# Kernel optimization log

Measured on AMD Instinct MI355X. Metric: run time of the kernel, lower is better.

Reference implementation:

```python
import jax, jax.numpy as jnp
import numpy as np

B, D0 = 1, 32
C = [32, 16, 16, 16]
DN = ('NDHWC', 'DHWIO', 'NDHWC')


def setup_inputs() -> dict:
    key = jax.random.key(0)
    ks = jax.random.split(key, 16)
    w = lambda k, s: jax.random.normal(k, s, jnp.float32) * 0.05
    occ0 = jax.random.bernoulli(ks[0], 0.3, (B, D0, D0, D0))
    x = jax.random.normal(ks[1], (B, D0, D0, D0, C[0]), jnp.float32) * occ0[..., None]
    gt0 = jax.random.bernoulli(ks[2], 0.3, (B, D0, D0, D0))
    gt1 = jax.random.bernoulli(ks[3], 0.3, (B, 2 * D0, 2 * D0, 2 * D0))
    gt2 = jax.random.bernoulli(ks[4], 0.3, (B, 4 * D0, 4 * D0, 4 * D0))
    return dict(
        x=x, occ0=occ0, gt0=gt0, gt1=gt1, gt2=gt2,
        w_conv0=w(ks[5], (3, 3, 3, C[0], C[1])), b_conv0=w(ks[6], (C[1],)),
        w_cls0=w(ks[7], (3, 3, 3, C[1], 1)), b_cls0=w(ks[8], (1,)),
        w_up1=w(ks[9], (2, 2, 2, C[1], C[2])), b_up1=w(ks[10], (C[2],)),
        w_conv1=w(ks[11], (3, 3, 3, C[2], C[2])), b_conv1=w(ks[12], (C[2],)),
        w_cls1=w(ks[13], (3, 3, 3, C[2], 1)), b_cls1=w(ks[14], (1,)),
        w_up2=w(jax.random.fold_in(key, 100), (2, 2, 2, C[2], C[3])), b_up2=w(jax.random.fold_in(key, 101), (C[3],)),
        w_conv2=w(jax.random.fold_in(key, 102), (3, 3, 3, C[3], C[3])), b_conv2=w(jax.random.fold_in(key, 103), (C[3],)),
        w_cls2=w(jax.random.fold_in(key, 104), (3, 3, 3, C[3], 1)), b_cls2=w(jax.random.fold_in(key, 105), (1,)),
        nums0=8192, nums1=32768, nums2=131072)


def conv3x3(x, w, b, occ):
    # stride-1 sparse conv == dense conv masked to existing coords
    y = jax.lax.conv_general_dilated(x, w, (1, 1, 1), 'SAME', dimension_numbers=DN)
    return (y + b) * occ[..., None].astype(y.dtype)


def up2x(x, w, b, occ):
    # generative transpose conv: every occupied voxel emits all 8 children
    y = jax.lax.conv_transpose(x, w, (2, 2, 2), 'VALID', dimension_numbers=DN)
    occ_up = jnp.repeat(jnp.repeat(jnp.repeat(occ, 2, 1), 2, 2), 2, 3)
    return (y + b) * occ_up[..., None].astype(y.dtype), occ_up


def prune(feats, occ, cls_logits, gt, k):
    # istopk over existing voxels, OR-ed with ground-truth membership (training=True)
    b = feats.shape[0]
    logits = jnp.where(occ, cls_logits[..., 0], -jnp.inf).reshape(b, -1)
    _, idx = jax.lax.top_k(logits, k)
    topk = jnp.zeros(logits.shape, bool).at[jnp.arange(b)[:, None], idx].set(True)
    mask = (topk.reshape(occ.shape) & occ) | (gt & occ)
    return feats * mask[..., None].astype(feats.dtype), mask


def hp_decoder(x, occ0, gt0, gt1, gt2,
               w_conv0, b_conv0, w_cls0, b_cls0,
               w_up1, b_up1, w_conv1, b_conv1, w_cls1, b_cls1,
               w_up2, b_up2, w_conv2, b_conv2, w_cls2, b_cls2,
               nums0, nums1, nums2):
    occ = occ0
    out = jax.nn.relu(conv3x3(x, w_conv0, b_conv0, occ))
    cls0 = conv3x3(out, w_cls0, b_cls0, occ)
    out, occ = prune(out, occ, cls0, gt0, nums0)
    h, occ = up2x(out, w_up1, b_up1, occ)
    out = jax.nn.relu(conv3x3(jax.nn.relu(h), w_conv1, b_conv1, occ))
    cls1 = conv3x3(out, w_cls1, b_cls1, occ)
    out, occ = prune(out, occ, cls1, gt1, nums1)
    h, occ = up2x(out, w_up2, b_up2, occ)
    out = jax.nn.relu(conv3x3(jax.nn.relu(h), w_conv2, b_conv2, occ))
    cls2 = conv3x3(out, w_cls2, b_cls2, occ)
    out, occ = prune(out, occ, cls2, gt2, nums2)
    return cls0, cls1, cls2, out


def reference(x, occ0, gt0, gt1, gt2,
              w_conv0, b_conv0, w_cls0, b_cls0,
              w_up1, b_up1, w_conv1, b_conv1, w_cls1, b_cls1,
              w_up2, b_up2, w_conv2, b_conv2, w_cls2, b_cls2,
              nums0, nums1, nums2):
    return hp_decoder(x, occ0, gt0, gt1, gt2,
                      w_conv0, b_conv0, w_cls0, b_cls0,
                      w_up1, b_up1, w_conv1, b_conv1, w_cls1, b_cls1,
                      w_up2, b_up2, w_conv2, b_conv2, w_cls2, b_cls2,
                      nums0, nums1, nums2)
```

## Files before the change

### kernel.cpp

```cpp
#include <hip/hip_runtime.h>
#include <stdint.h>


#define N0 32768
#define N1 262144
#define N2 2097152

#define OFF_CLS0 0L
#define OFF_CLS1 32768L
#define OFF_CLS2 294912L
#define OFF_OUT  2392064L

#define O_FLAGS 0UL
#define O_STATE 256UL
#define O_TIE   512UL
#define O_HIST1 66048UL
#define O_HIST2 328192UL
#define O_OCC0  590336UL
#define O_OCC1  623104UL
#define O_OCC2  885248UL
#define O_MASK0 2982400UL
#define O_MASK1 3015168UL
#define O_BCNT  3277312UL
#define O_SEL   5374464UL
#define O_KEYS  7471616UL
#define O_FEAT0 15860224UL
#define O_HR1   17957376UL
#define O_FEAT1 34734592UL
#define O_HR2   51511808UL
#define O_FEAT2 185729536UL

#define TIE_CAP 16000

__device__ __forceinline__ float ldf(const void* p, long i, int bf) {
    if (bf) {
        uint16_t h = ((const uint16_t*)p)[i];
        return __uint_as_float(((uint32_t)h) << 16);
    }
    return ((const float*)p)[i];
}
__device__ __forceinline__ int ldb(const void* p, long i, int m) {
    switch (m) {
        case 0: return ((const int*)p)[i] != 0;
        case 1: return ((const uint8_t*)p)[i] != 0;
        case 2: { uint16_t h = ((const uint16_t*)p)[i]; return (h & 0x7FFF) != 0; }
        case 4: return ((const long long*)p)[i] != 0;
        default: { float f = ((const float*)p)[i]; return f != 0.0f; }
    }
}
__device__ __forceinline__ float rndb(float f, int en) {
    if (!en) return f;
    uint32_t u = __float_as_uint(f);
    u += 0x7FFFu + ((u >> 16) & 1u);
    u &= 0xFFFF0000u;
    return __uint_as_float(u);
}
__device__ __forceinline__ void stf(void* p, long i, float v, int bf) {
    if (bf) {
        uint32_t u = __float_as_uint(v);
        u += 0x7FFFu + ((u >> 16) & 1u);
        ((uint16_t*)p)[i] = (uint16_t)(u >> 16);
    } else {
        ((float*)p)[i] = v;
    }
}
__device__ __forceinline__ uint32_t fkey(float f) {
    f = f + 0.0f;
    uint32_t u = __float_as_uint(f);
    return (u & 0x80000000u) ? ~u : (u | 0x80000000u);
}

__global__ void k_fzero(int* flags) {
    int t = threadIdx.x;
    if (t < 16) flags[8 + t] = 0;
}
__global__ void k_fscan(const void* x, const void* gt2, int* flags) {
    int* cnt = flags + 8;
    __shared__ int lc[8];
    int t = threadIdx.x;
    if (t < 8) lc[t] = 0;
    __syncthreads();
    long gid = (long)blockIdx.x * blockDim.x + threadIdx.x;
    long gstride = (long)gridDim.x * blockDim.x;
    int ltiny = 0;
    const uint32_t* xu = (const uint32_t*)x;
    for (long i = gid; i < 524288; i += gstride) {
        uint32_t u = xu[i];
        uint32_t e = (u >> 23) & 0xFFu;
        if (e == 0u && (u & 0x7FFFFFu) != 0u) ltiny++;
    }
    int l1off = 0, l1any = 0, l3f = 0, l84 = 0;
    const uint8_t* g = (const uint8_t*)gt2;
    for (long i = gid; i < 2097152; i += gstride) {
        uint8_t b = g[i];
        if (b == 1u) {
            l1any++;
            if ((i & 3) != 0) l1off++;
            if ((i & 7) == 4) l84++;
        }
        if (b == 0x3Fu && (i & 3) == 1) l3f++;
    }
    if (ltiny) atomicAdd(&lc[0], ltiny);
    if (l1off) atomicAdd(&lc[1], l1off);
    if (l1any) atomicAdd(&lc[2], l1any);
    if (l3f)   atomicAdd(&lc[3], l3f);
    if (l84)   atomicAdd(&lc[4], l84);
    __syncthreads();
    if (t < 5 && lc[t]) atomicAdd(&cnt[t], lc[t]);
}
__global__ void k_ffinal(int* flags) {
    if (threadIdx.x != 0 || blockIdx.x != 0) return;
    const int* cnt = flags + 8;
    flags[0] = (cnt[0] > 8) ? 1 : 0;
    int bm;
    if (cnt[1] > 8)       bm = 1;
    else if (cnt[2] > 8)  bm = (cnt[4] > 8) ? 0 : 4;
    else if (cnt[3] > 8)  bm = 2;
    else                  bm = 3;
    flags[1] = bm;
}

__global__ void k_zout(void* dout, long out_elems, const int* flags) {
    long bytes = out_elems * (flags[0] ? 2 : 4);
    long n16 = bytes >> 4;
    uint4 z = make_uint4(0, 0, 0, 0);
    uint4* p = (uint4*)dout;
    long stride = (long)gridDim.x * blockDim.x;
    for (long i = (long)blockIdx.x * blockDim.x + threadIdx.x; i < n16; i += stride)
        p[i] = z;
}

__global__ void k_xcast(const void* x, float* xf, const int* flags) {
    long i = (long)blockIdx.x * blockDim.x + threadIdx.x;
    if (i >= (long)N0 * 32) return;
    xf[i] = ldf(x, i, flags[0]);
}

__global__ void k_occ0cnt(const void* occraw, uint8_t* occ, const int* flags,
                          int* __restrict__ bcnt, uint8_t* maskz) {
    long v = (long)blockIdx.x * 256 + threadIdx.x;
    int a = (v < N0) ? ldb(occraw, v, flags[1]) : 0;
    if (v < N0) { occ[v] = (uint8_t)a; maskz[v] = 0; }
    unsigned long long m = __ballot(a != 0);
    __shared__ int wsum[4];
    int lane = threadIdx.x & 63, wid = threadIdx.x >> 6;
    if (lane == 0) wsum[wid] = (int)__popcll(m);
    __syncthreads();
    if (threadIdx.x == 0)
        bcnt[blockIdx.x] = wsum[0] + wsum[1] + wsum[2] + wsum[3];
}
template <int Dp>
__global__ void k_expcnt(const uint8_t* __restrict__ maskp, uint8_t* __restrict__ occc,
                         int* __restrict__ bcnt, uint8_t* maskz) {
    const int D = Dp * 2;
    long v = (long)blockIdx.x * 256 + threadIdx.x;
    const long N = (long)D * D * D;
    int a = 0;
    if (v < N) {
        int wd = (int)(v % D), hh = (int)((v / D) % D), dd = (int)(v / ((long)D * D));
        a = maskp[((long)(dd >> 1) * Dp + (hh >> 1)) * Dp + (wd >> 1)];
        occc[v] = (uint8_t)a;
        if (maskz) maskz[v] = 0;
    }
    unsigned long long m = __ballot(a != 0);
    __shared__ int wsum[4];
    int lane = threadIdx.x & 63, wid = threadIdx.x >> 6;
    if (lane == 0) wsum[wid] = (int)__popcll(m);
    __syncthreads();
    if (threadIdx.x == 0)
        bcnt[blockIdx.x] = wsum[0] + wsum[1] + wsum[2] + wsum[3];
}
__global__ void k_scanb(int* __restrict__ bcnt, int nb, int* cnt) {
    __shared__ int tsum[256];
    __shared__ int tpre[257];
    int t = threadIdx.x;
    int ch = (nb + 255) / 256;
    int lo = t * ch, hi = min(lo + ch, nb);
    int s = 0;
    for (int i = lo; i < hi; i++) s += bcnt[i];
    tsum[t] = s;
    __syncthreads();
    if (t == 0) {
        int run = 0;
        for (int j = 0; j < 256; j++) { tpre[j] = run; run += tsum[j]; }
        tpre[256] = run;
        cnt[0] = run;
    }
    __syncthreads();
    int run = tpre[t];
    for (int i = lo; i < hi; i++) { int x = bcnt[i]; bcnt[i] = run; run += x; }
}
__global__ void k_fill(const uint8_t* __restrict__ occ, long N,
                       const int* __restrict__ bcnt, int* __restrict__ list,
                       uint32_t* __restrict__ h1z) {
    long v = (long)blockIdx.x * 256 + threadIdx.x;
    for (long j = v; j < 65536; j += (long)gridDim.x * 256) h1z[j] = 0u;
    int a = (v < N) && occ[v];
    unsigned long long m = __ballot(a != 0);
    __shared__ int wsum[4];
    int lane = threadIdx.x & 63, wid = threadIdx.x >> 6;
    if (lane == 0) wsum[wid] = (int)__popcll(m);
    __syncthreads();
    int base = bcnt[blockIdx.x];
    for (int w = 0; w < wid; w++) base += wsum[w];
    if (a) list[base + (int)__popcll(m & ((1ull << lane) - 1ull))] = (int)v;
}

template <int CIN, int D>
__global__ void k_sconv16(const float* __restrict__ xin, const void* w, const void* bias,
                          const uint8_t* __restrict__ occ, const int* __restrict__ list,
                          const int* __restrict__ cnt, float* __restrict__ out,
                          const int* __restrict__ flags) {
    __shared__ float wl[27 * CIN * 16 + 16];
    const int n = cnt[0];
    if (blockIdx.x * 128 >= n) return;
    const int bf = flags[0];
    for (int i = threadIdx.x; i < 27 * CIN * 16; i += 256) wl[i] = ldf(w, i, bf);
    if (threadIdx.x < 16) wl[27 * CIN * 16 + threadIdx.x] = ldf(bias, threadIdx.x, bf);
    __syncthreads();
    int gid = blockIdx.x * 256 + threadIdx.x;
    int i = gid >> 1;
    if (i >= n) return;
    const int half = gid & 1;
    int v = list[i];
    int wd = v % D, hh = (v / D) % D, dd = v / (D * D);
    uint32_t nbm = 0u;
    {
        int t = 0;
#pragma unroll
        for (int kd = 0; kd < 3; kd++)
#pragma unroll
            for (int kh = 0; kh < 3; kh++)
#pragma unroll
                for (int kw = 0; kw < 3; kw++, t++) {
                    int d2 = dd + kd - 1, h2 = hh + kh - 1, w2 = wd + kw - 1;
                    int ok = (int)((unsigned)d2 < (unsigned)D) &
                             (int)((unsigned)h2 < (unsigned)D) &
                             (int)((unsigned)w2 < (unsigned)D);
                    int nv = v + (kd - 1) * D * D + (kh - 1) * D + (kw - 1);
                    int nvc = ok ? nv : v;
                    nbm |= ((uint32_t)((int)occ[nvc] & ok)) << t;
                }
    }
    float acc[8];
#pragma unroll
    for (int co = 0; co < 8; co++) acc[co] = 0.0f;
    int t = 0;
    for (int kd = 0; kd < 3; kd++) {
        for (int kh = 0; kh < 3; kh++) {
            for (int kw = 0; kw < 3; kw++, t++) {
                if (!((nbm >> t) & 1u)) continue;
                long nv = (long)v + (kd - 1) * (D * D) + (kh - 1) * D + (kw - 1);
                const float4* xp = (const float4*)(xin + nv * CIN);
                const float* wp = &wl[((kd * 3 + kh) * 3 + kw) * CIN * 16 + half * 8];
#pragma unroll
                for (int c4 = 0; c4 < CIN / 4; c4++) {
                    float4 x4 = xp[c4];
                    const float* wq = wp + c4 * 64;
#pragma unroll
                    for (int co = 0; co < 8; co++) acc[co] += x4.x * wq[co];
#pragma unroll
                    for (int co = 0; co < 8; co++) acc[co] += x4.y * wq[16 + co];
#pragma unroll
                    for (int co = 0; co < 8; co++) acc[co] += x4.z * wq[32 + co];
#pragma unroll
                    for (int co = 0; co < 8; co++) acc[co] += x4.w * wq[48 + co];
                }
            }
        }
    }
    float* op = out + (long)v * 16 + half * 8;
    const float* bp = &wl[27 * CIN * 16 + half * 8];
#pragma unroll
    for (int co = 0; co < 8; co++) {
        float val = rndb(acc[co], bf);
        val = rndb(val + bp[co], bf);
        op[co] = fmaxf(val, 0.0f);
    }
}

template <int D>
__global__ void k_scls(const float* __restrict__ feat, const void* w, const void* bias,
                       const uint8_t* __restrict__ occ, const int* __restrict__ list,
                       const int* __restrict__ cnt, void* dout, long ooff,
                       uint32_t* __restrict__ keyl, const int* __restrict__ flags) {
    __shared__ float wl[27 * 16 + 1];
    const int n = cnt[0];
    if (blockIdx.x * 128 >= n) return;
    const int bf = flags[0];
    for (int i = threadIdx.x; i < 27 * 16; i += 256) wl[i] = ldf(w, i, bf);
    if (threadIdx.x == 0) wl[432] = ldf(bias, 0, bf);
    __syncthreads();
    int gid = blockIdx.x * 256 + threadIdx.x;
    int i = gid >> 1;
    if (i >= n) return;
    const int half = gid & 1;
    int v = list[i];
    int wd = v % D, hh = (v / D) % D, dd = v / (D * D);
    uint32_t nbm = 0u;
    {
        int t = 0;
#pragma unroll
        for (int kd = 0; kd < 3; kd++)
#pragma unroll
            for (int kh = 0; kh < 3; kh++)
#pragma unroll
                for (int kw = 0; kw < 3; kw++, t++) {
                    int d2 = dd + kd - 1, h2 = hh + kh - 1, w2 = wd + kw - 1;
                    int ok = (int)((unsigned)d2 < (unsigned)D) &
                             (int)((unsigned)h2 < (unsigned)D) &
                             (int)((unsigned)w2 < (unsigned)D);
                    int nv = v + (kd - 1) * D * D + (kh - 1) * D + (kw - 1);
                    int nvc = ok ? nv : v;
                    nbm |= ((uint32_t)((int)occ[nvc] & ok)) << t;
                }
    }
    float acc = 0.0f;
    int t = 0;
    for (int kd = 0; kd < 3; kd++) {
        for (int kh = 0; kh < 3; kh++) {
            for (int kw = 0; kw < 3; kw++, t++) {
                if ((t & 1) != half) continue;
                if (!((nbm >> t) & 1u)) continue;
                long nv = (long)v + (kd - 1) * (D * D) + (kh - 1) * D + (kw - 1);
                const float4* xp = (const float4*)(feat + nv * 16);
                const float* wp = &wl[((kd * 3 + kh) * 3 + kw) * 16];
                float4 a0 = xp[0], a1 = xp[1], a2 = xp[2], a3 = xp[3];
                acc += a0.x * wp[0] + a0.y * wp[1] + a0.z * wp[2] + a0.w * wp[3];
                acc += a1.x * wp[4] + a1.y * wp[5] + a1.z * wp[6] + a1.w * wp[7];
                acc += a2.x * wp[8] + a2.y * wp[9] + a2.z * wp[10] + a2.w * wp[11];
                acc += a3.x * wp[12] + a3.y * wp[13] + a3.z * wp[14] + a3.w * wp[15];
            }
        }
    }
    acc += __shfl_xor(acc, 1, 64);
    if (half == 0) {
        float val = rndb(acc, bf);
        val = rndb(val + wl[432], bf);
        stf(dout, ooff + v, val, bf);
        keyl[i] = fkey(val);
    }
}

template <int Dp>
__global__ void k_sup(const float* __restrict__ featp, const void* w, const void* bias,
                      const int* __restrict__ list, const int* __restrict__ cnt,
                      float* __restrict__ hrelu, const int* __restrict__ flags) {
    __shared__ float wl[2048 + 16];
    const int n = cnt[0];
    if (blockIdx.x * 256 >= n) return;
    const int bf = flags[0];
    for (int i = threadIdx.x; i < 2048; i += 256) wl[i] = ldf(w, i, bf);
    if (threadIdx.x < 16) wl[2048 + threadIdx.x] = ldf(bias, threadIdx.x, bf);
    __syncthreads();
    int i = blockIdx.x * 256 + threadIdx.x;
    if (i >= n) return;
    int v = list[i];
    const int D = Dp * 2;
    int wd = v % D, hh = (v / D) % D, dd = v / (D * D);
    const float4* xp = (const float4*)(featp +
        ((long)((dd >> 1) * Dp + (hh >> 1)) * Dp + (wd >> 1)) * 16);
    int a = 1 - (dd & 1), b2 = 1 - (hh & 1), c = 1 - (wd & 1);
    const float* wp = &wl[((a * 2 + b2) * 2 + c) * 256];
    float acc[16];
#pragma unroll
    for (int co = 0; co < 16; co++) acc[co] = 0.0f;
#pragma unroll
    for (int c4 = 0; c4 < 4; c4++) {
        float4 x4 = xp[c4];
        const float* wq = wp + c4 * 64;
#pragma unroll
        for (int co = 0; co < 16; co++) acc[co] += x4.x * wq[co];
#pragma unroll
        for (int co = 0; co < 16; co++) acc[co] += x4.y * wq[16 + co];
#pragma unroll
        for (int co = 0; co < 16; co++) acc[co] += x4.z * wq[32 + co];
#pragma unroll
        for (int co = 0; co < 16; co++) acc[co] += x4.w * wq[48 + co];
    }
    float* op = hrelu + (long)v * 16;
#pragma unroll
    for (int co = 0; co < 16; co++) {
        float val = rndb(acc[co], bf);
        val = rndb(val + wl[2048 + co], bf);
        op[co] = fmaxf(val, 0.0f);
    }
}

__global__ void k_hist1(const uint32_t* __restrict__ keyl, const int* cnt,
                        uint32_t* __restrict__ hist) {
    __shared__ uint32_t lh[32768];
    const int n = cnt[0];
    for (int j = threadIdx.x; j < 32768; j += 256) lh[j] = 0u;
    __syncthreads();
    const int stride = gridDim.x * 256;
    for (int i = blockIdx.x * 256 + threadIdx.x; i < n; i += stride) {
        uint32_t bin = keyl[i] >> 16;
        atomicAdd(&lh[bin >> 1], 1u << ((bin & 1u) << 4));
    }
    __syncthreads();
    for (int j = threadIdx.x; j < 32768; j += 256) {
        uint32_t p = lh[j];
        if (p) {
            uint32_t lo = p & 0xFFFFu, hi = p >> 16;
            if (lo) atomicAdd(&hist[2 * j], lo);
            if (hi) atomicAdd(&hist[2 * j + 1], hi);
        }
    }
}
__global__ void k_scan1(const uint32_t* hist, const void* kptr, const int* cnt,
                        int* state, uint32_t* hist2) {
    __shared__ uint32_t part[256];
    int t = threadIdx.x;
    uint32_t s = 0;
    for (int j = 0; j < 256; j++) s += hist[t * 256 + j];
    part[t] = s;
    for (int i = t; i < 65536; i += 256) hist2[i] = 0u;
    __syncthreads();
    if (t == 0) {
        uint32_t k = (uint32_t)((const int*)kptr)[0];
        uint32_t total = (uint32_t)cnt[0];
        if (k >= total) {
            state[0] = -1;
            state[3] = 0;
            state[4] = 0;
            state[5] = 0;
            return;
        }
        uint32_t cum = 0, cab = 0;
        int B = 0;
        for (int c = 255; c >= 0; c--) {
            if (cum + part[c] >= k) {
                uint32_t cc = cum;
                for (int b = c * 256 + 255; b >= c * 256; b--) {
                    uint32_t h = hist[b];
                    if (cc + h >= k) { B = b; cab = cc; break; }
                    cc += h;
                }
                break;
            }
            cum += part[c];
        }
        state[0] = B;
        state[1] = (int)cab;
        state[2] = (int)(k - cab);
    }
}
__global__ void k_hist2(const uint32_t* __restrict__ keyl, const int* cnt,
                        const int* state, uint32_t* __restrict__ hist2) {
    if (state[0] < 0) return;
    __shared__ uint32_t lh[32768];
    const int n = cnt[0];
    const int B = state[0];
    for (int j = threadIdx.x; j < 32768; j += 256) lh[j] = 0u;
    __syncthreads();
    const int stride = gridDim.x * 256;
    for (int i = blockIdx.x * 256 + threadIdx.x; i < n; i += stride) {
        uint32_t key = keyl[i];
        if ((int)(key >> 16) == B) {
            uint32_t bin = key & 0xFFFFu;
            atomicAdd(&lh[bin >> 1], 1u << ((bin & 1u) << 4));
        }
    }
    __syncthreads();
    for (int j = threadIdx.x; j < 32768; j += 256) {
        uint32_t p = lh[j];
        if (p) {
            uint32_t lo = p & 0xFFFFu, hi = p >> 16;
            if (lo) atomicAdd(&hist2[2 * j], lo);
            if (hi) atomicAdd(&hist2[2 * j + 1], hi);
        }
    }
}
__global__ void k_scan2(const uint32_t* hist2, int* state) {
    __shared__ uint32_t part[256];
    int t = threadIdx.x;
    if (state[0] < 0) return;
    uint32_t s = 0;
    for (int j = 0; j < 256; j++) s += hist2[t * 256 + j];
    part[t] = s;
    __syncthreads();
    if (t == 0) {
        uint32_t krem = (uint32_t)state[2];
        uint32_t cum = 0, cl = 0;
        int L = 0;
        for (int c = 255; c >= 0; c--) {
            if (cum + part[c] >= krem) {
                uint32_t cc = cum;
                for (int b = c * 256 + 255; b >= c * 256; b--) {
                    uint32_t h = hist2[b];
                    if (cc + h >= krem) { L = b; cl = cc; break; }
                    cc += h;
                }
                break;
            }
            cum += part[c];
        }
        uint32_t K = ((uint32_t)state[0] << 16) | (uint32_t)L;
        state[3] = (int)K;
        state[4] = (int)(krem - cl);
        state[5] = 0;
    }
}
__global__ void k_markm(const uint32_t* __restrict__ keyl, const int* __restrict__ list,
                        const int* cnt, int* state, const void* gt,
                        uint8_t* __restrict__ mask, int* tiel, const int* flags) {
    int n = cnt[0];
    int i = blockIdx.x * 256 + threadIdx.x;
    uint32_t K = (uint32_t)state[3];
    int v = 0, isTie = 0;
    if (i < n) {
        uint32_t key = keyl[i];
        v = list[i];
        mask[v] = (uint8_t)((key > K) || ldb(gt, v, flags[1]));
        isTie = (key == K && K != 0u);
    }
    unsigned long long m = __ballot(isTie != 0);
    if (m) {
        int lane = threadIdx.x & 63;
        int leader = __ffsll((unsigned long long)m) - 1;
        int base = 0;
        if (lane == leader) base = atomicAdd(&state[5], (int)__popcll(m));
        base = __shfl(base, leader, 64);
        if (isTie) {
            int pos = base + (int)__popcll(m & ((1ull << lane) - 1ull));
            if (pos < TIE_CAP) tiel[pos] = v;
        }
    }
}
__global__ void k_tiesm(const int* state, const int* tiel, uint8_t* mask) {
    __shared__ int lst[TIE_CAP];
    int T = state[5];
    if (T > TIE_CAP) T = TIE_CAP;
    int need = state[4];
    if (need <= 0 || T == 0) return;
    for (int i = threadIdx.x; i < T; i += blockDim.x) lst[i] = tiel[i];
    __syncthreads();
    for (int e = threadIdx.x; e < T; e += blockDim.x) {
        int idx = lst[e], r = 0;
        for (int j = 0; j < T; j++) r += (lst[j] < idx) ? 1 : 0;
        if (r < need) mask[idx] = 1;
    }
}
__global__ void k_marko(const uint32_t* __restrict__ keyl, const int* __restrict__ list,
                        const int* cnt, int* state, const void* gt,
                        const float* __restrict__ feat, void* dout, int* tiel,
                        const int* flags) {
    int n = cnt[0];
    int i = blockIdx.x * 256 + threadIdx.x;
    uint32_t K = (uint32_t)state[3];
    int v = 0, isTie = 0;
    const int bf = flags[0];
    if (i < n) {
        uint32_t key = keyl[i];
        v = list[i];
        if ((key > K) || ldb(gt, v, flags[1])) {
            long base = OFF_OUT + (long)v * 16;
            const float* fp = feat + (long)v * 16;
#pragma unroll
            for (int co = 0; co < 16; co++) stf(dout, base + co, fp[co], bf);
        }
        isTie = (key == K && K != 0u);
    }
    unsigned long long m = __ballot(isTie != 0);
    if (m) {
        int lane = threadIdx.x & 63;
        int leader = __ffsll((unsigned long long)m) - 1;
        int base = 0;
        if (lane == leader) base = atomicAdd(&state[5], (int)__popcll(m));
        base = __shfl(base, leader, 64);
        if (isTie) {
            int pos = base + (int)__popcll(m & ((1ull << lane) - 1ull));
            if (pos < TIE_CAP) tiel[pos] = v;
        }
    }
}
__global__ void k_tieso(const int* state, const int* tiel,
                        const float* __restrict__ feat, void* dout, const int* flags) {
    __shared__ int lst[TIE_CAP];
    int T = state[5];
    if (T > TIE_CAP) T = TIE_CAP;
    int need = state[4];
    if (need <= 0 || T == 0) return;
    const int bf = flags[0];
    for (int i = threadIdx.x; i < T; i += blockDim.x) lst[i] = tiel[i];
    __syncthreads();
    for (int e = threadIdx.x; e < T; e += blockDim.x) {
        int idx = lst[e], r = 0;
        for (int j = 0; j < T; j++) r += (lst[j] < idx) ? 1 : 0;
        if (r < need) {
            long base = OFF_OUT + (long)idx * 16;
            const float* fp = feat + (long)idx * 16;
            for (int co = 0; co < 16; co++) stf(dout, base + co, fp[co], bf);
        }
    }
}

extern "C" void kernel_launch(void* const* d_in, const int* in_sizes, int n_in,
                              void* d_out, int out_size, void* d_ws, size_t ws_size,
                              hipStream_t stream) {
    char* ws = (char*)d_ws;
    int* flags = (int*)(ws + O_FLAGS);
    int* cnt = flags + 32;
    int* state = (int*)(ws + O_STATE);
    int* tiel = (int*)(ws + O_TIE);
    uint32_t* h1 = (uint32_t*)(ws + O_HIST1);
    uint32_t* h2 = (uint32_t*)(ws + O_HIST2);
    uint8_t* occ0 = (uint8_t*)(ws + O_OCC0);
    uint8_t* occ1 = (uint8_t*)(ws + O_OCC1);
    uint8_t* occ2 = (uint8_t*)(ws + O_OCC2);
    uint8_t* mask0 = (uint8_t*)(ws + O_MASK0);
    uint8_t* mask1 = (uint8_t*)(ws + O_MASK1);
    int* bcnt = (int*)(ws + O_BCNT);
    uint32_t* keyl = (uint32_t*)(ws + O_KEYS);
    float* feat0 = (float*)(ws + O_FEAT0);
    float* hr1 = (float*)(ws + O_HR1);
    float* feat1 = (float*)(ws + O_FEAT1);
    float* hr2 = (float*)(ws + O_HR2);
    float* feat2 = (float*)(ws + O_FEAT2);
    int* list0 = (int*)(ws + O_HR1);
    int* list1 = (int*)(ws + O_HR2);
    int* list2 = (int*)(ws + O_HR1);
    float* xf = (float*)(ws + O_HR2 + (4UL << 20));

    k_fzero<<<1, 64, 0, stream>>>(flags);
    k_fscan<<<512, 256, 0, stream>>>(d_in[0], d_in[4], flags);
    k_ffinal<<<1, 64, 0, stream>>>(flags);
    k_zout<<<2048, 256, 0, stream>>>(d_out, (long)out_size, flags);
    k_xcast<<<(N0 * 32) / 256, 256, 0, stream>>>(d_in[0], xf, flags);

    k_occ0cnt<<<N0 / 256, 256, 0, stream>>>(d_in[1], occ0, flags, bcnt, mask0);
    k_scanb<<<1, 256, 0, stream>>>(bcnt, N0 / 256, cnt);
    k_fill<<<N0 / 256, 256, 0, stream>>>(occ0, N0, bcnt, list0, h1);
    k_sconv16<32, 32><<<(2 * N0) / 256, 256, 0, stream>>>(xf, d_in[5], d_in[6], occ0,
                                                          list0, cnt, feat0, flags);
    k_scls<32><<<(2 * N0) / 256, 256, 0, stream>>>(feat0, d_in[7], d_in[8], occ0, list0,
                                                   cnt, d_out, OFF_CLS0, keyl, flags);
    k_hist1<<<256, 256, 0, stream>>>(keyl, cnt, h1);
    k_scan1<<<1, 256, 0, stream>>>(h1, d_in[21], cnt, state, h2);
    k_hist2<<<256, 256, 0, stream>>>(keyl, cnt, state, h2);
    k_scan2<<<1, 256, 0, stream>>>(h2, state);
    k_markm<<<N0 / 256, 256, 0, stream>>>(keyl, list0, cnt, state, d_in[2], mask0,
                                          tiel, flags);
    k_tiesm<<<1, 1024, 0, stream>>>(state, tiel, mask0);

    k_expcnt<32><<<N1 / 256, 256, 0, stream>>>(mask0, occ1, bcnt, mask1);
    k_scanb<<<1, 256, 0, stream>>>(bcnt, N1 / 256, cnt);
    k_fill<<<N1 / 256, 256, 0, stream>>>(occ1, N1, bcnt, list1, h1);
    k_sup<32><<<N1 / 256, 256, 0, stream>>>(feat0, d_in[9], d_in[10], list1, cnt,
                                            hr1, flags);
    k_sconv16<16, 64><<<(2 * N1) / 256, 256, 0, stream>>>(hr1, d_in[11], d_in[12], occ1,
                                                          list1, cnt, feat1, flags);
    k_scls<64><<<(2 * N1) / 256, 256, 0, stream>>>(feat1, d_in[13], d_in[14], occ1,
                                                   list1, cnt, d_out, OFF_CLS1, keyl,
                                                   flags);
    k_hist1<<<256, 256, 0, stream>>>(keyl, cnt, h1);
    k_scan1<<<1, 256, 0, stream>>>(h1, d_in[22], cnt, state, h2);
    k_hist2<<<256, 256, 0, stream>>>(keyl, cnt, state, h2);
    k_scan2<<<1, 256, 0, stream>>>(h2, state);
    k_markm<<<N1 / 256, 256, 0, stream>>>(keyl, list1, cnt, state, d_in[3], mask1,
                                          tiel, flags);
    k_tiesm<<<1, 1024, 0, stream>>>(state, tiel, mask1);

    k_expcnt<64><<<N2 / 256, 256, 0, stream>>>(mask1, occ2, bcnt, (uint8_t*)0);
    k_scanb<<<1, 256, 0, stream>>>(bcnt, N2 / 256, cnt);
    k_fill<<<N2 / 256, 256, 0, stream>>>(occ2, N2, bcnt, list2, h1);
    k_sup<64><<<N2 / 256, 256, 0, stream>>>(feat1, d_in[15], d_in[16], list2, cnt,
                                            hr2, flags);
    k_sconv16<16, 128><<<(2 * N2) / 256, 256, 0, stream>>>(hr2, d_in[17], d_in[18],
                                                           occ2, list2, cnt, feat2,
                                                           flags);
    k_scls<128><<<(2 * N2) / 256, 256, 0, stream>>>(feat2, d_in[19], d_in[20], occ2,
                                                    list2, cnt, d_out, OFF_CLS2, keyl,
                                                    flags);
    k_hist1<<<256, 256, 0, stream>>>(keyl, cnt, h1);
    k_scan1<<<1, 256, 0, stream>>>(h1, d_in[23], cnt, state, h2);
    k_hist2<<<256, 256, 0, stream>>>(keyl, cnt, state, h2);
    k_scan2<<<1, 256, 0, stream>>>(h2, state);
    k_marko<<<N2 / 256, 256, 0, stream>>>(keyl, list2, cnt, state, d_in[4], feat2,
                                          d_out, tiel, flags);
    k_tieso<<<1, 1024, 0, stream>>>(state, tiel, feat2, d_out, flags);
}
```

Baseline: 868.6 us.

## Use bf16 MFMA for 16-channel sparse convs and store upsampled features as bf16

```diff
diff --git a/kernel.cpp b/kernel.cpp
--- a/kernel.cpp
+++ b/kernel.cpp
@@ -32,6 +32,9 @@
 
 #define TIE_CAP 16000
 
+typedef short frag_ab __attribute__((ext_vector_type(8)));
+typedef float frag_cd __attribute__((ext_vector_type(4)));
+
 __device__ __forceinline__ float ldf(const void* p, long i, int bf) {
     if (bf) {
         uint16_t h = ((const uint16_t*)p)[i];
@@ -210,7 +213,8 @@
 __global__ void k_sconv16(const float* __restrict__ xin, const void* w, const void* bias,
                           const uint8_t* __restrict__ occ, const int* __restrict__ list,
                           const int* __restrict__ cnt, float* __restrict__ out,
-                          const int* __restrict__ flags) {
+                          const int* __restrict__ flags, int skip_bf) {
+    if (skip_bf && flags[0]) return;
     __shared__ float wl[27 * CIN * 16 + 16];
     const int n = cnt[0];
     if (blockIdx.x * 128 >= n) return;
@@ -276,6 +280,80 @@
         float val = rndb(acc[co], bf);
         val = rndb(val + bp[co], bf);
         op[co] = fmaxf(val, 0.0f);
+    }
+}
+
+template <int D>
+__global__ void k_sconv16_mfma(const uint16_t* __restrict__ hrb, const void* w,
+                               const void* bias, const uint8_t* __restrict__ occ,
+                               const int* __restrict__ list, const int* __restrict__ cnt,
+                               float* __restrict__ out, const int* __restrict__ flags) {
+    if (!flags[0]) return;
+    const int n = cnt[0];
+    const int ntiles = (n + 15) >> 4;
+    if ((int)blockIdx.x * 4 >= ntiles) return;
+    __shared__ uint16_t wl[27 * 256];
+    const uint16_t* wg = (const uint16_t*)w;
+    for (int i = threadIdx.x; i < 27 * 256; i += 256) wl[i] = wg[i];
+    __syncthreads();
+    const int lane = (int)(threadIdx.x & 63);
+    const int hi = lane >> 5;
+    const int cin0 = ((lane >> 4) & 1) * 8;
+    const int co = lane & 15;
+    frag_ab bfr[14];
+#pragma unroll
+    for (int T = 0; T < 14; T++) {
+        frag_ab b = {0, 0, 0, 0, 0, 0, 0, 0};
+        int tap = 2 * T + hi;
+        if (tap < 27) {
+            const uint16_t* wp = wl + (tap * 16 + cin0) * 16 + co;
+#pragma unroll
+            for (int j = 0; j < 8; j++) b[j] = (short)wp[j * 16];
+        }
+        bfr[T] = b;
+    }
+    const float biasv =
+        __uint_as_float((uint32_t)((const uint16_t*)bias)[co] << 16);
+    const frag_ab zero8 = {0, 0, 0, 0, 0, 0, 0, 0};
+    const int wave = (int)((blockIdx.x * blockDim.x + threadIdx.x) >> 6);
+    const int nwav = (int)((gridDim.x * blockDim.x) >> 6);
+    for (int tile = wave; tile < ntiles; tile += nwav) {
+        const int base = tile << 4;
+        int idx = base + co;
+        int v = (idx < n) ? list[idx] : 0;
+        int wd = v % D, hh = (v / D) % D, dd = v / (D * D);
+        frag_cd acc = {0.0f, 0.0f, 0.0f, 0.0f};
+#pragma unroll
+        for (int T = 0; T < 14; T++) {
+            const int t0 = 2 * T, t1 = 2 * T + 1;
+            const int kd0c = t0 / 9 - 1, kh0c = (t0 / 3) % 3 - 1, kw0c = t0 % 3 - 1;
+            const int kd1c = (t1 < 27) ? t1 / 9 - 1 : (1 << 20);
+            const int kh1c = (t1 < 27) ? (t1 / 3) % 3 - 1 : 0;
+            const int kw1c = (t1 < 27) ? t1 % 3 - 1 : 0;
+            int kd = hi ? kd1c : kd0c;
+            int kh = hi ? kh1c : kh0c;
+            int kw = hi ? kw1c : kw0c;
+            int d2 = dd + kd, h2 = hh + kh, w2 = wd + kw;
+            int ok = (int)((unsigned)d2 < (unsigned)D) &
+                     (int)((unsigned)h2 < (unsigned)D) &
+                     (int)((unsigned)w2 < (unsigned)D);
+            int nv = ok ? (v + kd * D * D + kh * D + kw) : v;
+            int live = ok & (int)occ[nv];
+            frag_ab a = *(const frag_ab*)(hrb + (long)nv * 16 + cin0);
+            a = live ? a : zero8;
+            acc = __builtin_amdgcn_mfma_f32_16x16x32_bf16(a, bfr[T], acc, 0, 0, 0);
+        }
+        const int r0 = (lane >> 4) * 4;
+#pragma unroll
+        for (int r = 0; r < 4; r++) {
+            int i = base + r0 + r;
+            if (i < n) {
+                int vr = list[i];
+                float valf = rndb(acc[r], 1);
+                valf = rndb(valf + biasv, 1);
+                out[(long)vr * 16 + co] = fmaxf(valf, 0.0f);
+            }
+        }
     }
 }
 
@@ -378,12 +456,22 @@
 #pragma unroll
         for (int co = 0; co < 16; co++) acc[co] += x4.w * wq[48 + co];
     }
-    float* op = hrelu + (long)v * 16;
-#pragma unroll
-    for (int co = 0; co < 16; co++) {
-        float val = rndb(acc[co], bf);
-        val = rndb(val + wl[2048 + co], bf);
-        op[co] = fmaxf(val, 0.0f);
+    if (bf) {
+        uint16_t* op = (uint16_t*)hrelu + (long)v * 16;
+#pragma unroll
+        for (int co = 0; co < 16; co++) {
+            float val = rndb(acc[co], 1);
+            val = rndb(val + wl[2048 + co], 1);
+            val = fmaxf(val, 0.0f);
+            op[co] = (uint16_t)(__float_as_uint(val) >> 16);
+        }
+    } else {
+        float* op = hrelu + (long)v * 16;
+#pragma unroll
+        for (int co = 0; co < 16; co++) {
+            float val = acc[co] + wl[2048 + co];
+            op[co] = fmaxf(val, 0.0f);
+        }
     }
 }
 
@@ -402,9 +490,9 @@
     for (int j = threadIdx.x; j < 32768; j += 256) {
         uint32_t p = lh[j];
         if (p) {
-            uint32_t lo = p & 0xFFFFu, hi = p >> 16;
+            uint32_t lo = p & 0xFFFFu, hh = p >> 16;
             if (lo) atomicAdd(&hist[2 * j], lo);
-            if (hi) atomicAdd(&hist[2 * j + 1], hi);
+            if (hh) atomicAdd(&hist[2 * j + 1], hh);
         }
     }
 }
@@ -466,9 +554,9 @@
     for (int j = threadIdx.x; j < 32768; j += 256) {
         uint32_t p = lh[j];
         if (p) {
-            uint32_t lo = p & 0xFFFFu, hi = p >> 16;
+            uint32_t lo = p & 0xFFFFu, hh = p >> 16;
             if (lo) atomicAdd(&hist2[2 * j], lo);
-            if (hi) atomicAdd(&hist2[2 * j + 1], hi);
+            if (hh) atomicAdd(&hist2[2 * j + 1], hh);
         }
     }
 }
@@ -633,7 +721,7 @@
     k_scanb<<<1, 256, 0, stream>>>(bcnt, N0 / 256, cnt);
     k_fill<<<N0 / 256, 256, 0, stream>>>(occ0, N0, bcnt, list0, h1);
     k_sconv16<32, 32><<<(2 * N0) / 256, 256, 0, stream>>>(xf, d_in[5], d_in[6], occ0,
-                                                          list0, cnt, feat0, flags);
+                                                          list0, cnt, feat0, flags, 0);
     k_scls<32><<<(2 * N0) / 256, 256, 0, stream>>>(feat0, d_in[7], d_in[8], occ0, list0,
                                                    cnt, d_out, OFF_CLS0, keyl, flags);
     k_hist1<<<256, 256, 0, stream>>>(keyl, cnt, h1);
@@ -650,7 +738,10 @@
     k_sup<32><<<N1 / 256, 256, 0, stream>>>(feat0, d_in[9], d_in[10], list1, cnt,
                                             hr1, flags);
     k_sconv16<16, 64><<<(2 * N1) / 256, 256, 0, stream>>>(hr1, d_in[11], d_in[12], occ1,
-                                                          list1, cnt, feat1, flags);
+                                                          list1, cnt, feat1, flags, 1);
+    k_sconv16_mfma<64><<<1024, 256, 0, stream>>>((const uint16_t*)hr1, d_in[11],
+                                                 d_in[12], occ1, list1, cnt, feat1,
+                                                 flags);
     k_scls<64><<<(2 * N1) / 256, 256, 0, stream>>>(feat1, d_in[13], d_in[14], occ1,
                                                    list1, cnt, d_out, OFF_CLS1, keyl,
                                                    flags);
@@ -669,7 +760,10 @@
                                             hr2, flags);
     k_sconv16<16, 128><<<(2 * N2) / 256, 256, 0, stream>>>(hr2, d_in[17], d_in[18],
                                                            occ2, list2, cnt, feat2,
-                                                           flags);
+                                                           flags, 1);
+    k_sconv16_mfma<128><<<2048, 256, 0, stream>>>((const uint16_t*)hr2, d_in[17],
+                                                  d_in[18], occ2, list2, cnt, feat2,
+                                                  flags);
     k_scls<128><<<(2 * N2) / 256, 256, 0, stream>>>(feat2, d_in[19], d_in[20], occ2,
                                                     list2, cnt, d_out, OFF_CLS2, keyl,
                                                     flags);
```

After: 873.3 us. Within noise of the previous version (+0.5%).
